# Kernel optimization log

Hardware: AMD Instinct MI355X
Metric: run time of the kernel (lower is better)

Reference implementation:

```python
import jax, jax.numpy as jnp
import numpy as np
from jax import lax


def setup_inputs() -> dict:
    key = jax.random.key(0)
    k1, k2 = jax.random.split(key)
    x = jax.random.normal(k1, (32, 256, 56, 56), dtype=jnp.float32)
    # Conv2d(in=2, out=1, k=7) weight in OIHW layout, plus bias
    w = jax.random.normal(k2, (1, 2, 7, 7), dtype=jnp.float32) * 0.1
    b = jnp.zeros((1,), dtype=jnp.float32)
    return {"x": x, "w": w, "b": b}


def reference(x, w, b):
    # channel-wise mean and max pooling -> [N,1,H,W] each
    y_avg = jnp.mean(x, axis=1, keepdims=True)
    y_max = jnp.max(x, axis=1, keepdims=True)
    y = jnp.concatenate([y_avg, y_max], axis=1)  # [N,2,H,W]
    pad = (w.shape[-1] - 1) // 2
    y = lax.conv_general_dilated(
        y, w,
        window_strides=(1, 1),
        padding=[(pad, pad), (pad, pad)],
        dimension_numbers=("NCHW", "OIHW", "NCHW"),
    ) + b[None, :, None, None]  # [N,1,H,W]
    scale = jax.nn.sigmoid(y)
    return x * scale
```

## Files before the change

### kernel.cpp

```cpp
#include <hip/hip_runtime.h>
#include <math.h>

#define N_IMG 32
#define C_CH  256
#define H     56
#define W     56
#define HW    (H * W)
#define CHW   (C_CH * HW)
#define HW4   (HW / 4)
#define TOTAL4 (N_IMG * CHW / 4)

__global__ __launch_bounds__(256) void reduce_kernel(
    const float* __restrict__ x,
    float* __restrict__ avg_map,
    float* __restrict__ max_map)
{
    const int n   = blockIdx.y;
    const int tid = threadIdx.x;
    const int sub = tid >> 5;
    const int pos = tid & 31;
    const int p4  = blockIdx.x * 32 + pos;
    const bool active = (p4 < HW4);

    float4 s = make_float4(0.f, 0.f, 0.f, 0.f);
    float4 m = make_float4(-INFINITY, -INFINITY, -INFINITY, -INFINITY);

    if (active) {
        const float* px = x + (size_t)n * CHW + (size_t)(sub * 32) * HW + (size_t)p4 * 4;
        #pragma unroll 8
        for (int i = 0; i < 32; ++i) {
            float4 v = *reinterpret_cast<const float4*>(px + (size_t)i * HW);
            s.x += v.x; s.y += v.y; s.z += v.z; s.w += v.w;
            m.x = fmaxf(m.x, v.x); m.y = fmaxf(m.y, v.y);
            m.z = fmaxf(m.z, v.z); m.w = fmaxf(m.w, v.w);
        }
    }

    __shared__ float4 ssum[256];
    __shared__ float4 smax[256];
    ssum[tid] = s;
    smax[tid] = m;
    __syncthreads();

    if (tid < 32) {
        const int myp4 = blockIdx.x * 32 + tid;
        if (myp4 < HW4) {
            float4 a = ssum[tid];
            #pragma unroll
            for (int k = 1; k < 8; ++k) {
                float4 v = ssum[tid + k * 32];
                a.x += v.x; a.y += v.y; a.z += v.z; a.w += v.w;
            }
            const float inv = 1.0f / 256.0f;
            a.x *= inv; a.y *= inv; a.z *= inv; a.w *= inv;
            *reinterpret_cast<float4*>(avg_map + (size_t)n * HW + (size_t)myp4 * 4) = a;
        }
    } else if (tid < 64) {
        const int p = tid - 32;
        const int myp4 = blockIdx.x * 32 + p;
        if (myp4 < HW4) {
            float4 a = smax[p];
            #pragma unroll
            for (int k = 1; k < 8; ++k) {
                float4 v = smax[p + k * 32];
                a.x = fmaxf(a.x, v.x); a.y = fmaxf(a.y, v.y);
                a.z = fmaxf(a.z, v.z); a.w = fmaxf(a.w, v.w);
            }
            *reinterpret_cast<float4*>(max_map + (size_t)n * HW + (size_t)myp4 * 4) = a;
        }
    }
}

#define LDSW 62
__global__ __launch_bounds__(256) void conv_kernel(
    const float* __restrict__ avg_map,
    const float* __restrict__ max_map,
    const float* __restrict__ w,
    const float* __restrict__ b,
    float* __restrict__ scale)
{
    const int n  = blockIdx.y;
    const int ry = blockIdx.x;
    const int tid = threadIdx.x;

    __shared__ float s_in[2][14][LDSW];
    __shared__ float s_w[98];
    __shared__ float s_b;

    float* s_raw = &s_in[0][0][0];
    for (int e = tid; e < 2 * 14 * LDSW; e += 256) s_raw[e] = 0.0f;
    if (tid < 98) s_w[tid] = w[tid];
    if (tid == 0) s_b = b[0];
    __syncthreads();

    for (int e = tid; e < 2 * 14 * 56; e += 256) {
        const int ch  = e / (14 * 56);
        const int r   = (e / 56) % 14;
        const int col = e % 56;
        const int gr  = ry * 8 - 3 + r;
        if (gr >= 0 && gr < H) {
            const float* src = (ch == 0) ? avg_map : max_map;
            s_in[ch][r][col + 3] = src[(size_t)n * HW + gr * W + col];
        }
    }
    __syncthreads();

    for (int o = tid; o < 8 * 56; o += 256) {
        const int r   = o / 56;
        const int col = o % 56;
        float acc = s_b;
        #pragma unroll
        for (int ch = 0; ch < 2; ++ch)
            #pragma unroll
            for (int i = 0; i < 7; ++i)
                #pragma unroll
                for (int j = 0; j < 7; ++j)
                    acc = fmaf(s_in[ch][r + i][col + j], s_w[ch * 49 + i * 7 + j], acc);
        const float sc = 1.0f / (1.0f + expf(-acc));
        scale[(size_t)n * HW + (ry * 8 + r) * W + col] = sc;
    }
}

__global__ __launch_bounds__(256) void apply_kernel(
    const float* __restrict__ x,
    const float* __restrict__ scale,
    float* __restrict__ out)
{
    const unsigned stride = gridDim.x * 256u;
    for (unsigned i = blockIdx.x * 256u + threadIdx.x; i < TOTAL4; i += stride) {
        const unsigned n    = i / (CHW / 4);
        const unsigned rem  = i - n * (CHW / 4);
        const unsigned hw4  = rem % HW4;
        const float4 sc = *reinterpret_cast<const float4*>(scale + (size_t)n * HW + (size_t)hw4 * 4);
        float4 v = reinterpret_cast<const float4*>(x)[i];
        v.x *= sc.x; v.y *= sc.y; v.z *= sc.z; v.w *= sc.w;
        reinterpret_cast<float4*>(out)[i] = v;
    }
}

extern "C" void kernel_launch(void* const* d_in, const int* in_sizes, int n_in,
                              void* d_out, int out_size, void* d_ws, size_t ws_size,
                              hipStream_t stream)
{
    const float* x = (const float*)d_in[0];
    const float* w = (const float*)d_in[1];
    const float* b = (const float*)d_in[2];
    float* out = (float*)d_out;

    float* ws       = (float*)d_ws;
    float* avg_map  = ws;
    float* max_map  = ws + (size_t)N_IMG * HW;
    float* scale    = ws + (size_t)2 * N_IMG * HW;

    dim3 gA((HW4 + 31) / 32, N_IMG);
    reduce_kernel<<<gA, 256, 0, stream>>>(x, avg_map, max_map);

    dim3 gB(H / 8, N_IMG);
    conv_kernel<<<gB, 256, 0, stream>>>(avg_map, max_map, w, b, scale);

    apply_kernel<<<2048, 256, 0, stream>>>(x, scale, out);
}
```

Measured before the change: 205.7 us.

## Fuse conv+sigmoid with apply pass, one block per image row

Merges the conv/sigmoid kernel and the elementwise apply kernel into one kernel. Each block handles one image row: it computes 56 scale values into shared memory, then multiplies all 256 channels of that row. This removes the scale-map round trip through global memory and one kernel launch. In exchange, every block recomputes a small conv step that only 56 of its 256 threads work on, and each thread's accesses are 224-byte row segments strided by the channel plane rather than fully contiguous. The reduce loop is also fully unrolled.

```diff
diff --git a/kernel.cpp b/kernel.cpp
--- a/kernel.cpp
+++ b/kernel.cpp
@@ -8,7 +8,7 @@
 #define HW    (H * W)
 #define CHW   (C_CH * HW)
 #define HW4   (HW / 4)
-#define TOTAL4 (N_IMG * CHW / 4)
+#define W4    (W / 4)
 
 __global__ __launch_bounds__(256) void reduce_kernel(
     const float* __restrict__ x,
@@ -27,7 +27,7 @@
 
     if (active) {
         const float* px = x + (size_t)n * CHW + (size_t)(sub * 32) * HW + (size_t)p4 * 4;
-        #pragma unroll 8
+        #pragma unroll
         for (int i = 0; i < 32; ++i) {
             float4 v = *reinterpret_cast<const float4*>(px + (size_t)i * HW);
             s.x += v.x; s.y += v.y; s.z += v.z; s.w += v.w;
@@ -72,32 +72,35 @@
 }
 
 #define LDSW 62
-__global__ __launch_bounds__(256) void conv_kernel(
+__global__ __launch_bounds__(256) void conv_apply_kernel(
+    const float* __restrict__ x,
     const float* __restrict__ avg_map,
     const float* __restrict__ max_map,
     const float* __restrict__ w,
     const float* __restrict__ b,
-    float* __restrict__ scale)
+    float* __restrict__ out)
 {
-    const int n  = blockIdx.y;
-    const int ry = blockIdx.x;
+    const int n   = blockIdx.y;
+    const int row = blockIdx.x;
     const int tid = threadIdx.x;
 
-    __shared__ float s_in[2][14][LDSW];
+    __shared__ float s_in[2][7][LDSW];
     __shared__ float s_w[98];
     __shared__ float s_b;
+    __shared__ float s_scale[W];
 
     float* s_raw = &s_in[0][0][0];
-    for (int e = tid; e < 2 * 14 * LDSW; e += 256) s_raw[e] = 0.0f;
+    #pragma unroll
+    for (int e = tid; e < 2 * 7 * LDSW; e += 256) s_raw[e] = 0.0f;
     if (tid < 98) s_w[tid] = w[tid];
     if (tid == 0) s_b = b[0];
     __syncthreads();
 
-    for (int e = tid; e < 2 * 14 * 56; e += 256) {
-        const int ch  = e / (14 * 56);
-        const int r   = (e / 56) % 14;
-        const int col = e % 56;
-        const int gr  = ry * 8 - 3 + r;
+    for (int e = tid; e < 2 * 7 * W; e += 256) {
+        const int ch  = e / (7 * W);
+        const int r   = (e / W) % 7;
+        const int col = e % W;
+        const int gr  = row - 3 + r;
         if (gr >= 0 && gr < H) {
             const float* src = (ch == 0) ? avg_map : max_map;
             s_in[ch][r][col + 3] = src[(size_t)n * HW + gr * W + col];
@@ -105,9 +108,7 @@
     }
     __syncthreads();
 
-    for (int o = tid; o < 8 * 56; o += 256) {
-        const int r   = o / 56;
-        const int col = o % 56;
+    if (tid < W) {
         float acc = s_b;
         #pragma unroll
         for (int ch = 0; ch < 2; ++ch)
@@ -115,26 +116,25 @@
             for (int i = 0; i < 7; ++i)
                 #pragma unroll
                 for (int j = 0; j < 7; ++j)
-                    acc = fmaf(s_in[ch][r + i][col + j], s_w[ch * 49 + i * 7 + j], acc);
-        const float sc = 1.0f / (1.0f + expf(-acc));
-        scale[(size_t)n * HW + (ry * 8 + r) * W + col] = sc;
+                    acc = fmaf(s_in[ch][i][tid + j], s_w[ch * 49 + i * 7 + j], acc);
+        s_scale[tid] = 1.0f / (1.0f + expf(-acc));
     }
-}
+    __syncthreads();
 
-__global__ __launch_bounds__(256) void apply_kernel(
-    const float* __restrict__ x,
-    const float* __restrict__ scale,
-    float* __restrict__ out)
-{
-    const unsigned stride = gridDim.x * 256u;
-    for (unsigned i = blockIdx.x * 256u + threadIdx.x; i < TOTAL4; i += stride) {
-        const unsigned n    = i / (CHW / 4);
-        const unsigned rem  = i - n * (CHW / 4);
-        const unsigned hw4  = rem % HW4;
-        const float4 sc = *reinterpret_cast<const float4*>(scale + (size_t)n * HW + (size_t)hw4 * 4);
-        float4 v = reinterpret_cast<const float4*>(x)[i];
-        v.x *= sc.x; v.y *= sc.y; v.z *= sc.z; v.w *= sc.w;
-        reinterpret_cast<float4*>(out)[i] = v;
+    const float* xrow = x + (size_t)n * CHW + (size_t)row * W;
+    float*       orow = out + (size_t)n * CHW + (size_t)row * W;
+    #pragma unroll
+    for (int iter = 0; iter < 14; ++iter) {
+        const int e  = iter * 256 + tid;
+        const int c  = e / W4;
+        const int w4 = e - c * W4;
+        const size_t off = (size_t)c * HW + (size_t)w4 * 4;
+        float4 v = *reinterpret_cast<const float4*>(xrow + off);
+        v.x *= s_scale[w4 * 4 + 0];
+        v.y *= s_scale[w4 * 4 + 1];
+        v.z *= s_scale[w4 * 4 + 2];
+        v.w *= s_scale[w4 * 4 + 3];
+        *reinterpret_cast<float4*>(orow + off) = v;
     }
 }
 
@@ -147,16 +147,13 @@
     const float* b = (const float*)d_in[2];
     float* out = (float*)d_out;
 
-    float* ws       = (float*)d_ws;
-    float* avg_map  = ws;
-    float* max_map  = ws + (size_t)N_IMG * HW;
-    float* scale    = ws + (size_t)2 * N_IMG * HW;
+    float* ws      = (float*)d_ws;
+    float* avg_map = ws;
+    float* max_map = ws + (size_t)N_IMG * HW;
 
     dim3 gA((HW4 + 31) / 32, N_IMG);
     reduce_kernel<<<gA, 256, 0, stream>>>(x, avg_map, max_map);
 
-    dim3 gB(H / 8, N_IMG);
-    conv_kernel<<<gB, 256, 0, stream>>>(avg_map, max_map, w, b, scale);
-
-    apply_kernel<<<2048, 256, 0, stream>>>(x, scale, out);
+    dim3 gB(H, N_IMG);
+    conv_apply_kernel<<<gB, 256, 0, stream>>>(x, avg_map, max_map, w, b, out);
 }
```

Result: slower. 222.7 us (median of 2 runs) (+8.2%).
